# Optimization experiments

Measured on AMD Instinct MI355X. Metric: run time of the kernel, lower is better.

The kernel has to match this reference:

```python
import jax, jax.numpy as jnp
import numpy as np

KNN = 4
H = 0.03


def setup_inputs() -> dict:
    key = jax.random.key(0)
    pc = jax.random.normal(key, (8, 4096, 3), dtype=jnp.float32)  # [B, N, 3]
    return {"pc": pc}


def reference(pc) -> jnp.ndarray:
    sq = jnp.sum(pc * pc, axis=-1)  # [B, N]
    # dist[b, i, j] = || pc[b,i] - pc[b,j] ||^2
    dist = sq[:, :, None] + sq[:, None, :] - 2.0 * jnp.einsum("bid,bjd->bij", pc, pc)
    dist = jnp.maximum(dist, 0.0)
    # k nearest neighbors with offset=1 (skip self): take smallest KNN+1, drop the first
    neg_top, _ = jax.lax.top_k(-dist, KNN + 1)  # sorted descending -> distances ascending
    knn_dist = -neg_top[..., 1:]  # [B, N, KNN]
    weight = jnp.exp(-knn_dist / (H * H))
    loss = jnp.sum(-knn_dist * weight)
    return loss
```

## Files before the change

kernel.cpp:

```cpp
#include <hip/hip_runtime.h>
#include <math.h>

#define NPTS   4096
#define NB     8
#define TILE   128
#define NWAVES 16
#define BLK    (NWAVES * 64)
#define JCHUNK (NPTS / NWAVES)
#define INV_H2 (1.0f / (0.03f * 0.03f))
#define INFV   3.0e38f

__device__ __forceinline__ float med3f(float a, float b, float c) {
#if defined(__has_builtin)
#if __has_builtin(__builtin_amdgcn_fmed3f)
  return __builtin_amdgcn_fmed3f(a, b, c);
#else
  return fminf(c, fmaxf(a, b));
#endif
#else
  return fminf(c, fmaxf(a, b));
#endif
}

template <int CHECK>
__device__ __forceinline__ void scan2(const float4* __restrict__ sP, int lo, int hi,
                                      int self_lo, int self_hi,
                                      float mxl, float myl, float mzl,
                                      float mxh, float myh, float mzh,
                                      float& a0, float& a1, float& a2, float& a3,
                                      float& b0, float& b1, float& b2, float& b3) {
#pragma unroll 8
  for (int j = lo; j < hi; ++j) {
    float4 q = sP[j];
    float tl = fmaf(mzl, q.z, q.w);
    tl = fmaf(myl, q.y, tl);
    tl = fmaf(mxl, q.x, tl);
    float th = fmaf(mzh, q.z, q.w);
    th = fmaf(myh, q.y, th);
    th = fmaf(mxh, q.x, th);
    if (CHECK == 1) tl = (j == self_lo) ? INFV : tl;
    if (CHECK == 2) th = (j == self_hi) ? INFV : th;
    a3 = med3f(a2, tl, a3);
    a2 = med3f(a1, tl, a2);
    a1 = med3f(a0, tl, a1);
    a0 = fminf(a0, tl);
    b3 = med3f(b2, th, b3);
    b2 = med3f(b1, th, b2);
    b1 = med3f(b0, th, b1);
    b0 = fminf(b0, th);
  }
}

__device__ __forceinline__ void merge4(float a0, float a1, float a2, float a3,
                                       float b0, float b1, float b2, float b3,
                                       float& o0, float& o1, float& o2, float& o3) {
  float L0 = fminf(a0, b3), L1 = fminf(a1, b2), L2 = fminf(a2, b1), L3 = fminf(a3, b0);
  float e0 = fminf(L0, L2), e2 = fmaxf(L0, L2);
  float e1 = fminf(L1, L3), e3 = fmaxf(L1, L3);
  o0 = fminf(e0, e1); o1 = fmaxf(e0, e1);
  o2 = fminf(e2, e3); o3 = fmaxf(e2, e3);
}

__global__ __launch_bounds__(BLK)
void repulsion_kernel(const float* __restrict__ pc, float* __restrict__ out) {
  __shared__ float4 sP[NPTS];
  __shared__ float4 cand[NWAVES * TILE];

  const int blk  = blockIdx.x;
  const int b    = blk >> 5;
  const int tile = blk & 31;
  const int tid  = threadIdx.x;
  const float* base = pc + (size_t)b * NPTS * 3;
  const float4* pcv = (const float4*)base;

  {
    const int g = tid;
    float4 a = pcv[3 * g + 0];
    float4 c = pcv[3 * g + 1];
    float4 e = pcv[3 * g + 2];
    float x0 = a.x, y0 = a.y, z0 = a.z;
    float x1 = a.w, y1 = c.x, z1 = c.y;
    float x2 = c.z, y2 = c.w, z2 = e.x;
    float x3 = e.y, y3 = e.z, z3 = e.w;
    sP[4 * g + 0] = make_float4(x0, y0, z0, fmaf(x0, x0, fmaf(y0, y0, z0 * z0)));
    sP[4 * g + 1] = make_float4(x1, y1, z1, fmaf(x1, x1, fmaf(y1, y1, z1 * z1)));
    sP[4 * g + 2] = make_float4(x2, y2, z2, fmaf(x2, x2, fmaf(y2, y2, z2 * z2)));
    sP[4 * g + 3] = make_float4(x3, y3, z3, fmaf(x3, x3, fmaf(y3, y3, z3 * z3)));
  }
  __syncthreads();

  const int w    = tid >> 6;
  const int lane = tid & 63;
  const int self_lo = tile * TILE + lane;
  const int self_hi = self_lo + 64;

  float4 plo = sP[self_lo];
  float4 phi = sP[self_hi];
  const float mxl = -2.0f * plo.x, myl = -2.0f * plo.y, mzl = -2.0f * plo.z;
  const float mxh = -2.0f * phi.x, myh = -2.0f * phi.y, mzh = -2.0f * phi.z;

  float a0 = INFV, a1 = INFV, a2 = INFV, a3 = INFV;
  float b0 = INFV, b1 = INFV, b2 = INFV, b3 = INFV;

  const int j0 = w * JCHUNK;
  const int cs = tile >> 1;
  if (w == cs) {
    const int s = j0 + ((tile & 1) << 7);
    scan2<0>(sP, j0, s, self_lo, self_hi, mxl, myl, mzl, mxh, myh, mzh,
             a0, a1, a2, a3, b0, b1, b2, b3);
    scan2<1>(sP, s, s + 64, self_lo, self_hi, mxl, myl, mzl, mxh, myh, mzh,
             a0, a1, a2, a3, b0, b1, b2, b3);
    scan2<2>(sP, s + 64, s + 128, self_lo, self_hi, mxl, myl, mzl, mxh, myh, mzh,
             a0, a1, a2, a3, b0, b1, b2, b3);
    scan2<0>(sP, s + 128, j0 + JCHUNK, self_lo, self_hi, mxl, myl, mzl, mxh, myh, mzh,
             a0, a1, a2, a3, b0, b1, b2, b3);
  } else {
    scan2<0>(sP, j0, j0 + JCHUNK, self_lo, self_hi, mxl, myl, mzl, mxh, myh, mzh,
             a0, a1, a2, a3, b0, b1, b2, b3);
  }

  cand[w * TILE + lane]      = make_float4(a0, a1, a2, a3);
  cand[w * TILE + 64 + lane] = make_float4(b0, b1, b2, b3);
  __syncthreads();

  if (tid < TILE) {
    float4 M = cand[tid];
    float m0 = M.x, m1 = M.y, m2 = M.z, m3 = M.w;
#pragma unroll
    for (int ww = 1; ww < NWAVES; ++ww) {
      float4 Cw = cand[ww * TILE + tid];
      merge4(m0, m1, m2, m3, Cw.x, Cw.y, Cw.z, Cw.w, m0, m1, m2, m3);
    }

    const float sqi = sP[tile * TILE + tid].w;
    float d0 = fmaxf(m0 + sqi, 0.0f);
    float d1 = fmaxf(m1 + sqi, 0.0f);
    float d2 = fmaxf(m2 + sqi, 0.0f);
    float d3 = fmaxf(m3 + sqi, 0.0f);

    float s = 0.0f;
    s -= d0 * expf(-d0 * INV_H2);
    s -= d1 * expf(-d1 * INV_H2);
    s -= d2 * expf(-d2 * INV_H2);
    s -= d3 * expf(-d3 * INV_H2);

    for (int off = 32; off > 0; off >>= 1) s += __shfl_down(s, off);
    if (lane == 0) atomicAdd(out, s);
  }
}

extern "C" void kernel_launch(void* const* d_in, const int* in_sizes, int n_in,
                              void* d_out, int out_size, void* d_ws, size_t ws_size,
                              hipStream_t stream) {
  const float* pc = (const float*)d_in[0];
  float* out = (float*)d_out;
  hipMemsetAsync(out, 0, sizeof(float), stream);
  repulsion_kernel<<<dim3(NB * (NPTS / TILE)), dim3(BLK), 0, stream>>>(pc, out);
}
```

Measured before the change: 82.22 us.

## Register-block four query points per lane and split candidate scan across halves

Each lane now tracks top-4 for four query points instead of two, so every shared-memory load of a candidate point is reused across more queries. The candidate range is split into two halves handled by separate blocks, keeping the grid size at 256 blocks. Per-half results go to workspace and a second finalize kernel merges them and computes the exp-weighted sum. This raises register pressure and adds a kernel launch and a global round trip. The merge stage now handles 256 queries per block with only a quarter of the threads active.

```diff
diff --git a/kernel.cpp b/kernel.cpp
--- a/kernel.cpp
+++ b/kernel.cpp
@@ -3,10 +3,14 @@
 
 #define NPTS   4096
 #define NB     8
-#define TILE   128
+#define IR     4
+#define TILE   (64 * IR)
+#define NTILE  (NPTS / TILE)
 #define NWAVES 16
 #define BLK    (NWAVES * 64)
-#define JCHUNK (NPTS / NWAVES)
+#define NHALF  2
+#define JHALF  (NPTS / NHALF)
+#define JCHUNK (JHALF / NWAVES)
 #define INV_H2 (1.0f / (0.03f * 0.03f))
 #define INFV   3.0e38f
 
@@ -22,32 +26,23 @@
 #endif
 }
 
-template <int CHECK>
-__device__ __forceinline__ void scan2(const float4* __restrict__ sP, int lo, int hi,
-                                      int self_lo, int self_hi,
-                                      float mxl, float myl, float mzl,
-                                      float mxh, float myh, float mzh,
-                                      float& a0, float& a1, float& a2, float& a3,
-                                      float& b0, float& b1, float& b2, float& b3) {
-#pragma unroll 8
+template <bool CHECK>
+__device__ __forceinline__ void scan4(const float4* __restrict__ sP, int lo, int hi,
+                                      const int self[IR],
+                                      const float mx[IR], const float my[IR],
+                                      const float mz[IR], float t[IR][4]) {
+#pragma unroll 4
   for (int j = lo; j < hi; ++j) {
     float4 q = sP[j];
-    float tl = fmaf(mzl, q.z, q.w);
-    tl = fmaf(myl, q.y, tl);
-    tl = fmaf(mxl, q.x, tl);
-    float th = fmaf(mzh, q.z, q.w);
-    th = fmaf(myh, q.y, th);
-    th = fmaf(mxh, q.x, th);
-    if (CHECK == 1) tl = (j == self_lo) ? INFV : tl;
-    if (CHECK == 2) th = (j == self_hi) ? INFV : th;
-    a3 = med3f(a2, tl, a3);
-    a2 = med3f(a1, tl, a2);
-    a1 = med3f(a0, tl, a1);
-    a0 = fminf(a0, tl);
-    b3 = med3f(b2, th, b3);
-    b2 = med3f(b1, th, b2);
-    b1 = med3f(b0, th, b1);
-    b0 = fminf(b0, th);
+#pragma unroll
+    for (int k = 0; k < IR; ++k) {
+      float d = fmaf(mx[k], q.x, fmaf(my[k], q.y, fmaf(mz[k], q.z, q.w)));
+      if (CHECK) d = (j == self[k]) ? INFV : d;
+      t[k][3] = med3f(t[k][2], d, t[k][3]);
+      t[k][2] = med3f(t[k][1], d, t[k][2]);
+      t[k][1] = med3f(t[k][0], d, t[k][1]);
+      t[k][0] = fminf(t[k][0], d);
+    }
   }
 }
 
@@ -62,16 +57,17 @@
 }
 
 __global__ __launch_bounds__(BLK)
-void repulsion_kernel(const float* __restrict__ pc, float* __restrict__ out) {
+void repulsion_scan(const float* __restrict__ pc, float4* __restrict__ ws) {
   __shared__ float4 sP[NPTS];
   __shared__ float4 cand[NWAVES * TILE];
 
   const int blk  = blockIdx.x;
   const int b    = blk >> 5;
-  const int tile = blk & 31;
+  const int r    = blk & 31;
+  const int tile = r >> 1;
+  const int h    = r & 1;
   const int tid  = threadIdx.x;
-  const float* base = pc + (size_t)b * NPTS * 3;
-  const float4* pcv = (const float4*)base;
+  const float4* pcv = (const float4*)(pc + (size_t)b * NPTS * 3);
 
   {
     const int g = tid;
@@ -91,36 +87,27 @@
 
   const int w    = tid >> 6;
   const int lane = tid & 63;
-  const int self_lo = tile * TILE + lane;
-  const int self_hi = self_lo + 64;
 
-  float4 plo = sP[self_lo];
-  float4 phi = sP[self_hi];
-  const float mxl = -2.0f * plo.x, myl = -2.0f * plo.y, mzl = -2.0f * plo.z;
-  const float mxh = -2.0f * phi.x, myh = -2.0f * phi.y, mzh = -2.0f * phi.z;
-
-  float a0 = INFV, a1 = INFV, a2 = INFV, a3 = INFV;
-  float b0 = INFV, b1 = INFV, b2 = INFV, b3 = INFV;
-
-  const int j0 = w * JCHUNK;
-  const int cs = tile >> 1;
-  if (w == cs) {
-    const int s = j0 + ((tile & 1) << 7);
-    scan2<0>(sP, j0, s, self_lo, self_hi, mxl, myl, mzl, mxh, myh, mzh,
-             a0, a1, a2, a3, b0, b1, b2, b3);
-    scan2<1>(sP, s, s + 64, self_lo, self_hi, mxl, myl, mzl, mxh, myh, mzh,
-             a0, a1, a2, a3, b0, b1, b2, b3);
-    scan2<2>(sP, s + 64, s + 128, self_lo, self_hi, mxl, myl, mzl, mxh, myh, mzh,
-             a0, a1, a2, a3, b0, b1, b2, b3);
-    scan2<0>(sP, s + 128, j0 + JCHUNK, self_lo, self_hi, mxl, myl, mzl, mxh, myh, mzh,
-             a0, a1, a2, a3, b0, b1, b2, b3);
-  } else {
-    scan2<0>(sP, j0, j0 + JCHUNK, self_lo, self_hi, mxl, myl, mzl, mxh, myh, mzh,
-             a0, a1, a2, a3, b0, b1, b2, b3);
+  int   self[IR];
+  float mx[IR], my[IR], mz[IR], t[IR][4];
+#pragma unroll
+  for (int k = 0; k < IR; ++k) {
+    self[k] = tile * TILE + 64 * k + lane;
+    float4 p = sP[self[k]];
+    mx[k] = -2.0f * p.x; my[k] = -2.0f * p.y; mz[k] = -2.0f * p.z;
+    t[k][0] = INFV; t[k][1] = INFV; t[k][2] = INFV; t[k][3] = INFV;
   }
 
-  cand[w * TILE + lane]      = make_float4(a0, a1, a2, a3);
-  cand[w * TILE + 64 + lane] = make_float4(b0, b1, b2, b3);
+  const int j0 = h * JHALF + w * JCHUNK;
+  const bool check = (h == (tile >> 3)) && ((w >> 1) == (tile & 7));
+  if (check)
+    scan4<true >(sP, j0, j0 + JCHUNK, self, mx, my, mz, t);
+  else
+    scan4<false>(sP, j0, j0 + JCHUNK, self, mx, my, mz, t);
+
+#pragma unroll
+  for (int k = 0; k < IR; ++k)
+    cand[w * TILE + 64 * k + lane] = make_float4(t[k][0], t[k][1], t[k][2], t[k][3]);
   __syncthreads();
 
   if (tid < TILE) {
@@ -131,21 +118,50 @@
       float4 Cw = cand[ww * TILE + tid];
       merge4(m0, m1, m2, m3, Cw.x, Cw.y, Cw.z, Cw.w, m0, m1, m2, m3);
     }
+    ws[((size_t)(b * NTILE + tile) * NHALF + h) * TILE + tid] =
+        make_float4(m0, m1, m2, m3);
+  }
+}
 
-    const float sqi = sP[tile * TILE + tid].w;
-    float d0 = fmaxf(m0 + sqi, 0.0f);
-    float d1 = fmaxf(m1 + sqi, 0.0f);
-    float d2 = fmaxf(m2 + sqi, 0.0f);
-    float d3 = fmaxf(m3 + sqi, 0.0f);
+__global__ __launch_bounds__(TILE)
+void repulsion_finalize(const float* __restrict__ pc, const float4* __restrict__ ws,
+                        float* __restrict__ out) {
+  const int blk  = blockIdx.x;
+  const int b    = blk >> 4;
+  const int tile = blk & 15;
+  const int tid  = threadIdx.x;
 
-    float s = 0.0f;
-    s -= d0 * expf(-d0 * INV_H2);
-    s -= d1 * expf(-d1 * INV_H2);
-    s -= d2 * expf(-d2 * INV_H2);
-    s -= d3 * expf(-d3 * INV_H2);
+  const size_t base = (size_t)(b * NTILE + tile) * NHALF;
+  float4 A = ws[(base + 0) * TILE + tid];
+  float4 B = ws[(base + 1) * TILE + tid];
+  float m0, m1, m2, m3;
+  merge4(A.x, A.y, A.z, A.w, B.x, B.y, B.z, B.w, m0, m1, m2, m3);
 
-    for (int off = 32; off > 0; off >>= 1) s += __shfl_down(s, off);
-    if (lane == 0) atomicAdd(out, s);
+  const float* p = pc + ((size_t)b * NPTS + tile * TILE + tid) * 3;
+  const float px = p[0], py = p[1], pz = p[2];
+  const float sqi = fmaf(px, px, fmaf(py, py, pz * pz));
+
+  float d0 = fmaxf(m0 + sqi, 0.0f);
+  float d1 = fmaxf(m1 + sqi, 0.0f);
+  float d2 = fmaxf(m2 + sqi, 0.0f);
+  float d3 = fmaxf(m3 + sqi, 0.0f);
+
+  float s = 0.0f;
+  s -= d0 * expf(-d0 * INV_H2);
+  s -= d1 * expf(-d1 * INV_H2);
+  s -= d2 * expf(-d2 * INV_H2);
+  s -= d3 * expf(-d3 * INV_H2);
+
+  for (int off = 32; off > 0; off >>= 1) s += __shfl_down(s, off);
+
+  __shared__ float wsum[TILE / 64];
+  if ((tid & 63) == 0) wsum[tid >> 6] = s;
+  __syncthreads();
+  if (tid == 0) {
+    float tot = 0.0f;
+#pragma unroll
+    for (int i = 0; i < TILE / 64; ++i) tot += wsum[i];
+    atomicAdd(out, tot);
   }
 }
 
@@ -154,6 +170,8 @@
                               hipStream_t stream) {
   const float* pc = (const float*)d_in[0];
   float* out = (float*)d_out;
+  float4* ws = (float4*)d_ws;
   hipMemsetAsync(out, 0, sizeof(float), stream);
-  repulsion_kernel<<<dim3(NB * (NPTS / TILE)), dim3(BLK), 0, stream>>>(pc, out);
+  repulsion_scan<<<dim3(NB * NTILE * NHALF), dim3(BLK), 0, stream>>>(pc, ws);
+  repulsion_finalize<<<dim3(NB * NTILE), dim3(TILE), 0, stream>>>(pc, ws, out);
 }
```

Measured after the change: 83.92 us. 1.02x slower.
